# Kernel tuning notes

Hardware: AMD Instinct MI355X
Metric: run time of the kernel (lower is better)

Reference implementation:

```python
import jax, jax.numpy as jnp
import numpy as np

NODE_NUM = 256  # nodes per env block; N = NODE_NUM * n_thr
N, MAX_DEG, N_FEAT, N_HID, N_CLASS = 8192, 16, 128, 256, 64


def _xavier_uniform(key, fan_in, fan_out, gain=1.414):
    limit = gain * np.sqrt(6.0 / (fan_in + fan_out))
    return jax.random.uniform(key, (fan_in, fan_out), jnp.float32, -limit, limit)


def setup_inputs() -> dict:
    key = jax.random.key(0)
    k1, k2, k3, k4 = jax.random.split(key, 4)
    x = jax.random.normal(k1, (N, N_FEAT), jnp.float32)
    edge_index = jax.random.randint(k2, (N, MAX_DEG), 0, NODE_NUM)  # local neighbor ids, -1 = pad
    W1 = _xavier_uniform(k3, N_FEAT, N_HID)
    W2 = _xavier_uniform(k4, N_HID, N_CLASS)
    return {"x": x, "edge_index": edge_index, "W1": W1, "W2": W2}


def build_adj(edge_index, node_num):
    # Vectorized version of the nested-Python-loop to_adj scatter.
    n, d = edge_index.shape
    rows = jnp.broadcast_to(jnp.arange(n)[:, None], (n, d))  # [N, D]
    cols = edge_index + node_num * (rows // node_num)        # global neighbor index
    valid = (edge_index != -1).astype(jnp.float32)
    # .max with 0 for invalid entries is a no-op regardless of the (wrapped) index,
    # exactly reproducing "set adj[i, j_ind] = 1 only when j != -1".
    adj = jnp.zeros((n, n), jnp.float32).at[rows.ravel(), cols.ravel()].max(valid.ravel())
    return adj


def reference(x, edge_index, W1, W2):
    adj = build_adj(edge_index, NODE_NUM)            # [N, N]
    h = jax.nn.relu(adj @ (x @ W1))                  # gc1 + relu (dropout is identity at eval)
    out = adj @ (h @ W2)                             # gc2
    return jax.nn.log_softmax(out, axis=1)
```

## Files before the change

### kernel.cpp

```cpp
#include <hip/hip_runtime.h>
#include <math.h>

#define NNODES   8192
#define NODE_NUM 256
#define MAX_DEG  16
#define N_FEAT   128
#define N_HID    256
#define N_CLASS  64

#define AG_STRIDE 136
#define HB_STRIDE 264

typedef __attribute__((ext_vector_type(8))) short bf16x8;
typedef __attribute__((ext_vector_type(4))) float f32x4;

static __device__ __forceinline__ short f2b(float f) {
    unsigned u = __float_as_uint(f);
    unsigned r = (u + 0x7fffu + ((u >> 16) & 1u)) >> 16;
    return (short)r;
}

__global__ __launch_bounds__(512) void k_main(const float* __restrict__ x,
                                              const int* __restrict__ edge,
                                              const float* __restrict__ W1,
                                              const float* __restrict__ W2,
                                              unsigned int* __restrict__ maskw,
                                              float* __restrict__ t2) {
    __shared__ short agg[32 * AG_STRIDE];
    __shared__ short hb[32 * HB_STRIDE];

    const int bid  = blockIdx.x;
    const int work = (bid & 7) * 32 + (bid >> 3);
    const int row0 = work * 32;
    const int t    = threadIdx.x;
    const int w    = t >> 6, l = t & 63;
    const int l16  = l & 15, l4 = l >> 4;

    bf16x8 w1f[4][4];
    {
        const int ntb = (w & 3) * 4;
#pragma unroll
        for (int n = 0; n < 4; ++n)
#pragma unroll
            for (int k4 = 0; k4 < 4; ++k4) {
                const int col = (ntb + n) * 16 + l16;
                const int kb  = k4 * 32 + l4 * 8;
                bf16x8 v;
#pragma unroll
                for (int j = 0; j < 8; ++j) v[j] = f2b(W1[(kb + j) * N_HID + col]);
                w1f[n][k4] = v;
            }
    }
    bf16x8 w2f[8];
    {
        const int col = (w & 3) * 16 + l16;
#pragma unroll
        for (int k8 = 0; k8 < 8; ++k8) {
            const int kb = k8 * 32 + l4 * 8;
            bf16x8 v;
#pragma unroll
            for (int j = 0; j < 8; ++j) v[j] = f2b(W2[(kb + j) * N_CLASS + col]);
            w2f[k8] = v;
        }
    }

    {
        const int r = t >> 4, c = t & 15;
        const int node = row0 + r;
        const int base = node & ~(NODE_NUM - 1);
        const int* e = edge + (size_t)node * MAX_DEG;
        int ids[MAX_DEG];
#pragma unroll
        for (int k = 0; k < MAX_DEG; ++k) ids[k] = e[k];
        unsigned m = 0;
#pragma unroll
        for (int k = 0; k < MAX_DEG; ++k) {
            bool skip = (ids[k] == -1);
#pragma unroll
            for (int q = 0; q < k; ++q) skip = skip || (ids[q] == ids[k]);
            if (!skip) m |= 1u << k;
        }
        if (c == 0) maskw[node] = m;
        float a[8] = {0, 0, 0, 0, 0, 0, 0, 0};
#pragma unroll
        for (int k = 0; k < MAX_DEG; ++k) {
            if (m & (1u << k)) {
                const float* rowp = x + (size_t)(base + ids[k]) * N_FEAT + c * 8;
                float4 v0 = *(const float4*)(rowp);
                float4 v1 = *(const float4*)(rowp + 4);
                a[0] += v0.x; a[1] += v0.y; a[2] += v0.z; a[3] += v0.w;
                a[4] += v1.x; a[5] += v1.y; a[6] += v1.z; a[7] += v1.w;
            }
        }
        bf16x8 p;
#pragma unroll
        for (int j = 0; j < 8; ++j) p[j] = f2b(a[j]);
        *(bf16x8*)(&agg[r * AG_STRIDE + c * 8]) = p;
    }
    __syncthreads();

    const int mt = w >> 2, ntc = w & 3;
    {
        bf16x8 af[4];
#pragma unroll
        for (int k4 = 0; k4 < 4; ++k4)
            af[k4] = *(const bf16x8*)(&agg[(mt * 16 + l16) * AG_STRIDE + k4 * 32 + l4 * 8]);
#pragma unroll
        for (int n = 0; n < 4; ++n) {
            f32x4 acc = {0.f, 0.f, 0.f, 0.f};
#pragma unroll
            for (int k4 = 0; k4 < 4; ++k4)
                acc = __builtin_amdgcn_mfma_f32_16x16x32_bf16(af[k4], w1f[n][k4], acc, 0, 0, 0);
#pragma unroll
            for (int r = 0; r < 4; ++r)
                hb[(mt * 16 + l4 * 4 + r) * HB_STRIDE + (ntc * 4 + n) * 16 + l16] =
                    f2b(fmaxf(acc[r], 0.f));
        }
    }
    __syncthreads();

    {
        f32x4 acc = {0.f, 0.f, 0.f, 0.f};
#pragma unroll
        for (int k8 = 0; k8 < 8; ++k8) {
            bf16x8 a = *(const bf16x8*)(&hb[(mt * 16 + l16) * HB_STRIDE + k8 * 32 + l4 * 8]);
            acc = __builtin_amdgcn_mfma_f32_16x16x32_bf16(a, w2f[k8], acc, 0, 0, 0);
        }
#pragma unroll
        for (int r = 0; r < 4; ++r)
            t2[(size_t)(row0 + mt * 16 + l4 * 4 + r) * N_CLASS + ntc * 16 + l16] = acc[r];
    }
}

__global__ __launch_bounds__(512) void k_final(const float* __restrict__ t2,
                                               const int* __restrict__ edge,
                                               const unsigned int* __restrict__ maskw,
                                               float* __restrict__ out) {
    const int bid  = blockIdx.x;
    const int work = (bid & 7) * 32 + (bid >> 3);
    const int row0 = work * 32;
    const int t    = threadIdx.x;
    const int r = t >> 4, c = t & 15;
    const int node = row0 + r;
    const int base = node & ~(NODE_NUM - 1);
    const int* e = edge + (size_t)node * MAX_DEG;
    const unsigned m = maskw[node];

    float4 acc = {0.f, 0.f, 0.f, 0.f};
#pragma unroll
    for (int k = 0; k < MAX_DEG; ++k) {
        if (m & (1u << k)) {
            float4 v = *(const float4*)(t2 + (size_t)(base + e[k]) * N_CLASS + c * 4);
            acc.x += v.x; acc.y += v.y; acc.z += v.z; acc.w += v.w;
        }
    }
    float mx = fmaxf(fmaxf(acc.x, acc.y), fmaxf(acc.z, acc.w));
#pragma unroll
    for (int o = 1; o < 16; o <<= 1) mx = fmaxf(mx, __shfl_xor(mx, o, 64));
    float s = expf(acc.x - mx) + expf(acc.y - mx) + expf(acc.z - mx) + expf(acc.w - mx);
#pragma unroll
    for (int o = 1; o < 16; o <<= 1) s += __shfl_xor(s, o, 64);
    const float lse = mx + logf(s);

    float4 o4 = {acc.x - lse, acc.y - lse, acc.z - lse, acc.w - lse};
    *(float4*)(out + (size_t)node * N_CLASS + c * 4) = o4;
}

extern "C" void kernel_launch(void* const* d_in, const int* in_sizes, int n_in,
                              void* d_out, int out_size, void* d_ws, size_t ws_size,
                              hipStream_t stream) {
    const float* x    = (const float*)d_in[0];
    const int*   edge = (const int*)d_in[1];
    const float* W1   = (const float*)d_in[2];
    const float* W2   = (const float*)d_in[3];
    float* out = (float*)d_out;

    char* ws = (char*)d_ws;
    unsigned int* maskw = (unsigned int*)ws;
    float*        t2    = (float*)(ws + (64 << 10));

    k_main <<<NNODES / 32, 512, 0, stream>>>(x, edge, W1, W2, maskw, t2);
    k_final<<<NNODES / 32, 512, 0, stream>>>(t2, edge, maskw, out);
}
```

Baseline: 79.22 us.

## Pre-pack bf16 weight fragments and masks in a prep kernel, store t2 as bf16

Adds a prep kernel that computes the neighbor dedup masks and converts W1/W2 into bf16 MFMA fragment layout once. Each main-kernel block then loads its weight fragments with vector loads instead of strided scalar fp32 loads plus per-element conversion. The intermediate t2 is stored in bf16, halving its traffic, and the final kernel gathers 8 bf16 values per thread. The cost is an extra kernel launch and serialization between kernels, plus reduced precision in t2.

```diff
diff --git a/kernel.cpp b/kernel.cpp
--- a/kernel.cpp
+++ b/kernel.cpp
@@ -19,13 +19,48 @@
     unsigned r = (u + 0x7fffu + ((u >> 16) & 1u)) >> 16;
     return (short)r;
 }
-
-__global__ __launch_bounds__(512) void k_main(const float* __restrict__ x,
-                                              const int* __restrict__ edge,
+static __device__ __forceinline__ float b2f(short s) {
+    return __uint_as_float(((unsigned)(unsigned short)s) << 16);
+}
+
+__global__ __launch_bounds__(256) void k_prep(const int* __restrict__ edge,
                                               const float* __restrict__ W1,
                                               const float* __restrict__ W2,
                                               unsigned int* __restrict__ maskw,
-                                              float* __restrict__ t2) {
+                                              short* __restrict__ W1T,
+                                              short* __restrict__ W2T) {
+    const int g = blockIdx.x * 256 + threadIdx.x;
+    if (g < 8192) {
+        const int* e = edge + (size_t)g * MAX_DEG;
+        int ids[MAX_DEG];
+#pragma unroll
+        for (int k = 0; k < MAX_DEG; ++k) ids[k] = e[k];
+        unsigned m = 0;
+#pragma unroll
+        for (int k = 0; k < MAX_DEG; ++k) {
+            bool skip = (ids[k] == -1);
+#pragma unroll
+            for (int q = 0; q < k; ++q) skip = skip || (ids[q] == ids[k]);
+            if (!skip) m |= 1u << k;
+        }
+        maskw[g] = m;
+    } else if (g < 40960) {
+        const int o = g - 8192;
+        const int j = o & 7, l = (o >> 3) & 63, k4 = (o >> 9) & 3, nt = (o >> 11) & 15;
+        W1T[o] = f2b(W1[(k4 * 32 + (l >> 4) * 8 + j) * N_HID + nt * 16 + (l & 15)]);
+    } else if (g < 57344) {
+        const int o = g - 40960;
+        const int j = o & 7, l = (o >> 3) & 63, k8 = (o >> 9) & 7, nt = (o >> 12) & 3;
+        W2T[o] = f2b(W2[(k8 * 32 + (l >> 4) * 8 + j) * N_CLASS + nt * 16 + (l & 15)]);
+    }
+}
+
+__global__ __launch_bounds__(512) void k_main(const float* __restrict__ x,
+                                              const int* __restrict__ edge,
+                                              const unsigned int* __restrict__ maskw,
+                                              const short* __restrict__ W1T,
+                                              const short* __restrict__ W2T,
+                                              short* __restrict__ t2b) {
     __shared__ short agg[32 * AG_STRIDE];
     __shared__ short hb[32 * HB_STRIDE];
 
@@ -42,26 +77,15 @@
 #pragma unroll
         for (int n = 0; n < 4; ++n)
 #pragma unroll
-            for (int k4 = 0; k4 < 4; ++k4) {
-                const int col = (ntb + n) * 16 + l16;
-                const int kb  = k4 * 32 + l4 * 8;
-                bf16x8 v;
-#pragma unroll
-                for (int j = 0; j < 8; ++j) v[j] = f2b(W1[(kb + j) * N_HID + col]);
-                w1f[n][k4] = v;
-            }
+            for (int k4 = 0; k4 < 4; ++k4)
+                w1f[n][k4] = *(const bf16x8*)(W1T + ((size_t)((ntb + n) * 4 + k4) * 64 + l) * 8);
     }
     bf16x8 w2f[8];
     {
-        const int col = (w & 3) * 16 + l16;
-#pragma unroll
-        for (int k8 = 0; k8 < 8; ++k8) {
-            const int kb = k8 * 32 + l4 * 8;
-            bf16x8 v;
-#pragma unroll
-            for (int j = 0; j < 8; ++j) v[j] = f2b(W2[(kb + j) * N_CLASS + col]);
-            w2f[k8] = v;
-        }
+        const int nt = w & 3;
+#pragma unroll
+        for (int k8 = 0; k8 < 8; ++k8)
+            w2f[k8] = *(const bf16x8*)(W2T + ((size_t)(nt * 8 + k8) * 64 + l) * 8);
     }
 
     {
@@ -69,23 +93,12 @@
         const int node = row0 + r;
         const int base = node & ~(NODE_NUM - 1);
         const int* e = edge + (size_t)node * MAX_DEG;
-        int ids[MAX_DEG];
-#pragma unroll
-        for (int k = 0; k < MAX_DEG; ++k) ids[k] = e[k];
-        unsigned m = 0;
-#pragma unroll
-        for (int k = 0; k < MAX_DEG; ++k) {
-            bool skip = (ids[k] == -1);
-#pragma unroll
-            for (int q = 0; q < k; ++q) skip = skip || (ids[q] == ids[k]);
-            if (!skip) m |= 1u << k;
-        }
-        if (c == 0) maskw[node] = m;
+        const unsigned m = maskw[node];
         float a[8] = {0, 0, 0, 0, 0, 0, 0, 0};
 #pragma unroll
         for (int k = 0; k < MAX_DEG; ++k) {
             if (m & (1u << k)) {
-                const float* rowp = x + (size_t)(base + ids[k]) * N_FEAT + c * 8;
+                const float* rowp = x + (size_t)(base + e[k]) * N_FEAT + c * 8;
                 float4 v0 = *(const float4*)(rowp);
                 float4 v1 = *(const float4*)(rowp + 4);
                 a[0] += v0.x; a[1] += v0.y; a[2] += v0.z; a[3] += v0.w;
@@ -128,11 +141,11 @@
         }
 #pragma unroll
         for (int r = 0; r < 4; ++r)
-            t2[(size_t)(row0 + mt * 16 + l4 * 4 + r) * N_CLASS + ntc * 16 + l16] = acc[r];
-    }
-}
-
-__global__ __launch_bounds__(512) void k_final(const float* __restrict__ t2,
+            t2b[(size_t)(row0 + mt * 16 + l4 * 4 + r) * N_CLASS + ntc * 16 + l16] = f2b(acc[r]);
+    }
+}
+
+__global__ __launch_bounds__(256) void k_final(const short* __restrict__ t2b,
                                                const int* __restrict__ edge,
                                                const unsigned int* __restrict__ maskw,
                                                float* __restrict__ out) {
@@ -140,30 +153,38 @@
     const int work = (bid & 7) * 32 + (bid >> 3);
     const int row0 = work * 32;
     const int t    = threadIdx.x;
-    const int r = t >> 4, c = t & 15;
+    const int r = t >> 3, mm = t & 7;
     const int node = row0 + r;
     const int base = node & ~(NODE_NUM - 1);
     const int* e = edge + (size_t)node * MAX_DEG;
     const unsigned m = maskw[node];
 
-    float4 acc = {0.f, 0.f, 0.f, 0.f};
+    float acc[8] = {0, 0, 0, 0, 0, 0, 0, 0};
 #pragma unroll
     for (int k = 0; k < MAX_DEG; ++k) {
         if (m & (1u << k)) {
-            float4 v = *(const float4*)(t2 + (size_t)(base + e[k]) * N_CLASS + c * 4);
-            acc.x += v.x; acc.y += v.y; acc.z += v.z; acc.w += v.w;
-        }
-    }
-    float mx = fmaxf(fmaxf(acc.x, acc.y), fmaxf(acc.z, acc.w));
-#pragma unroll
-    for (int o = 1; o < 16; o <<= 1) mx = fmaxf(mx, __shfl_xor(mx, o, 64));
-    float s = expf(acc.x - mx) + expf(acc.y - mx) + expf(acc.z - mx) + expf(acc.w - mx);
-#pragma unroll
-    for (int o = 1; o < 16; o <<= 1) s += __shfl_xor(s, o, 64);
+            bf16x8 v = *(const bf16x8*)(t2b + (size_t)(base + e[k]) * N_CLASS + mm * 8);
+#pragma unroll
+            for (int j = 0; j < 8; ++j) acc[j] += b2f(v[j]);
+        }
+    }
+    float mx = acc[0];
+#pragma unroll
+    for (int j = 1; j < 8; ++j) mx = fmaxf(mx, acc[j]);
+#pragma unroll
+    for (int o = 1; o < 8; o <<= 1) mx = fmaxf(mx, __shfl_xor(mx, o, 64));
+    float s = 0.f;
+#pragma unroll
+    for (int j = 0; j < 8; ++j) s += expf(acc[j] - mx);
+#pragma unroll
+    for (int o = 1; o < 8; o <<= 1) s += __shfl_xor(s, o, 64);
     const float lse = mx + logf(s);
 
-    float4 o4 = {acc.x - lse, acc.y - lse, acc.z - lse, acc.w - lse};
-    *(float4*)(out + (size_t)node * N_CLASS + c * 4) = o4;
+    float* op = out + (size_t)node * N_CLASS + mm * 8;
+    float4 o0 = {acc[0] - lse, acc[1] - lse, acc[2] - lse, acc[3] - lse};
+    float4 o1 = {acc[4] - lse, acc[5] - lse, acc[6] - lse, acc[7] - lse};
+    *(float4*)(op)     = o0;
+    *(float4*)(op + 4) = o1;
 }
 
 extern "C" void kernel_launch(void* const* d_in, const int* in_sizes, int n_in,
@@ -177,8 +198,11 @@
 
     char* ws = (char*)d_ws;
     unsigned int* maskw = (unsigned int*)ws;
-    float*        t2    = (float*)(ws + (64 << 10));
-
-    k_main <<<NNODES / 32, 512, 0, stream>>>(x, edge, W1, W2, maskw, t2);
-    k_final<<<NNODES / 32, 512, 0, stream>>>(t2, edge, maskw, out);
-}
+    short*        W1T   = (short*)(ws + (32 << 10));
+    short*        W2T   = (short*)(ws + (96 << 10));
+    short*        t2b   = (short*)(ws + (128 << 10));
+
+    k_prep <<<256,         256, 0, stream>>>(edge, W1, W2, maskw, W1T, W2T);
+    k_main <<<NNODES / 32, 512, 0, stream>>>(x, edge, maskw, W1T, W2T, t2b);
+    k_final<<<NNODES / 32, 256, 0, stream>>>(t2b, edge, maskw, out);
+}
```

Result: faster. 77.26 us (-2.5%).

## Fuse both GCN kernels with per-env grid barrier and bf16 intermediate

Applied to the files above, without the earlier changes.

Merges the two kernels into one, where the eight blocks of each 256-node env synchronize through an atomic counter barrier before the second aggregation and log-softmax. W1 and W2 are staged through LDS with coalesced float4 loads instead of strided global gathers, and the intermediate t2 is stored as bf16 to halve gather traffic. This removes the second launch and the mask round-trip. In exchange it adds a memset, relies on all blocks of an env being co-resident to avoid deadlock, and loses some precision in t2.

```diff
diff --git a/kernel.cpp b/kernel.cpp
--- a/kernel.cpp
+++ b/kernel.cpp
@@ -12,6 +12,7 @@
 #define HB_STRIDE 264
 
 typedef __attribute__((ext_vector_type(8))) short bf16x8;
+typedef __attribute__((ext_vector_type(4))) short s16x4;
 typedef __attribute__((ext_vector_type(4))) float f32x4;
 
 static __device__ __forceinline__ short f2b(float f) {
@@ -19,60 +20,41 @@
     unsigned r = (u + 0x7fffu + ((u >> 16) & 1u)) >> 16;
     return (short)r;
 }
-
-__global__ __launch_bounds__(512) void k_main(const float* __restrict__ x,
-                                              const int* __restrict__ edge,
-                                              const float* __restrict__ W1,
-                                              const float* __restrict__ W2,
-                                              unsigned int* __restrict__ maskw,
-                                              float* __restrict__ t2) {
-    __shared__ short agg[32 * AG_STRIDE];
-    __shared__ short hb[32 * HB_STRIDE];
+static __device__ __forceinline__ float b2f(short s) {
+    return __uint_as_float(((unsigned)(unsigned short)s) << 16);
+}
+
+__global__ __launch_bounds__(512) void k_one(const float* __restrict__ x,
+                                             const int* __restrict__ edge,
+                                             const float* __restrict__ W1,
+                                             const float* __restrict__ W2,
+                                             short* __restrict__ t2b,
+                                             unsigned int* __restrict__ bar,
+                                             float* __restrict__ out) {
+    __shared__ __align__(16) char smem[131072];
+    float* w1s = (float*)smem;
+    float* w2s = (float*)smem;
+    short* agg = (short*)smem;
+    short* hb  = (short*)(smem + 32 * AG_STRIDE * 2);
 
     const int bid  = blockIdx.x;
     const int work = (bid & 7) * 32 + (bid >> 3);
     const int row0 = work * 32;
+    const int env  = work >> 3;
     const int t    = threadIdx.x;
     const int w    = t >> 6, l = t & 63;
     const int l16  = l & 15, l4 = l >> 4;
 
-    bf16x8 w1f[4][4];
+    const int r = t >> 4, c = t & 15;
+    const int node = row0 + r;
+    const int base = node & ~(NODE_NUM - 1);
+    const int* e = edge + (size_t)node * MAX_DEG;
+
+    unsigned m = 0;
     {
-        const int ntb = (w & 3) * 4;
-#pragma unroll
-        for (int n = 0; n < 4; ++n)
-#pragma unroll
-            for (int k4 = 0; k4 < 4; ++k4) {
-                const int col = (ntb + n) * 16 + l16;
-                const int kb  = k4 * 32 + l4 * 8;
-                bf16x8 v;
-#pragma unroll
-                for (int j = 0; j < 8; ++j) v[j] = f2b(W1[(kb + j) * N_HID + col]);
-                w1f[n][k4] = v;
-            }
-    }
-    bf16x8 w2f[8];
-    {
-        const int col = (w & 3) * 16 + l16;
-#pragma unroll
-        for (int k8 = 0; k8 < 8; ++k8) {
-            const int kb = k8 * 32 + l4 * 8;
-            bf16x8 v;
-#pragma unroll
-            for (int j = 0; j < 8; ++j) v[j] = f2b(W2[(kb + j) * N_CLASS + col]);
-            w2f[k8] = v;
-        }
-    }
-
-    {
-        const int r = t >> 4, c = t & 15;
-        const int node = row0 + r;
-        const int base = node & ~(NODE_NUM - 1);
-        const int* e = edge + (size_t)node * MAX_DEG;
         int ids[MAX_DEG];
 #pragma unroll
         for (int k = 0; k < MAX_DEG; ++k) ids[k] = e[k];
-        unsigned m = 0;
 #pragma unroll
         for (int k = 0; k < MAX_DEG; ++k) {
             bool skip = (ids[k] == -1);
@@ -80,7 +62,6 @@
             for (int q = 0; q < k; ++q) skip = skip || (ids[q] == ids[k]);
             if (!skip) m |= 1u << k;
         }
-        if (c == 0) maskw[node] = m;
         float a[8] = {0, 0, 0, 0, 0, 0, 0, 0};
 #pragma unroll
         for (int k = 0; k < MAX_DEG; ++k) {
@@ -92,78 +73,121 @@
                 a[4] += v1.x; a[5] += v1.y; a[6] += v1.z; a[7] += v1.w;
             }
         }
-        bf16x8 p;
-#pragma unroll
-        for (int j = 0; j < 8; ++j) p[j] = f2b(a[j]);
-        *(bf16x8*)(&agg[r * AG_STRIDE + c * 8]) = p;
+
+        {
+            const float4* s4 = (const float4*)W1;
+            float4* d4 = (float4*)w1s;
+#pragma unroll
+            for (int i = 0; i < 16; ++i) d4[i * 512 + t] = s4[i * 512 + t];
+        }
+        __syncthreads();
+        bf16x8 w1f[4][4];
+        {
+            const int ntb = (w & 3) * 4;
+#pragma unroll
+            for (int n = 0; n < 4; ++n)
+#pragma unroll
+                for (int k4 = 0; k4 < 4; ++k4) {
+                    bf16x8 v;
+#pragma unroll
+                    for (int j = 0; j < 8; ++j)
+                        v[j] = f2b(w1s[(k4 * 32 + l4 * 8 + j) * N_HID + (ntb + n) * 16 + l16]);
+                    w1f[n][k4] = v;
+                }
+        }
+        __syncthreads();
+        {
+            const float4* s4 = (const float4*)W2;
+            float4* d4 = (float4*)w2s;
+#pragma unroll
+            for (int i = 0; i < 8; ++i) d4[i * 512 + t] = s4[i * 512 + t];
+        }
+        __syncthreads();
+        bf16x8 w2f[8];
+        {
+            const int nt = w & 3;
+#pragma unroll
+            for (int k8 = 0; k8 < 8; ++k8) {
+                bf16x8 v;
+#pragma unroll
+                for (int j = 0; j < 8; ++j)
+                    v[j] = f2b(w2s[(k8 * 32 + l4 * 8 + j) * N_CLASS + nt * 16 + l16]);
+                w2f[k8] = v;
+            }
+        }
+        __syncthreads();
+
+        {
+            bf16x8 p;
+#pragma unroll
+            for (int j = 0; j < 8; ++j) p[j] = f2b(a[j]);
+            *(bf16x8*)(agg + r * AG_STRIDE + c * 8) = p;
+        }
+        __syncthreads();
+
+        const int mt = w >> 2, ntc = w & 3;
+        {
+            bf16x8 af[4];
+#pragma unroll
+            for (int k4 = 0; k4 < 4; ++k4)
+                af[k4] = *(const bf16x8*)(agg + (mt * 16 + l16) * AG_STRIDE + k4 * 32 + l4 * 8);
+#pragma unroll
+            for (int n = 0; n < 4; ++n) {
+                f32x4 acc = {0.f, 0.f, 0.f, 0.f};
+#pragma unroll
+                for (int k4 = 0; k4 < 4; ++k4)
+                    acc = __builtin_amdgcn_mfma_f32_16x16x32_bf16(af[k4], w1f[n][k4], acc, 0, 0, 0);
+#pragma unroll
+                for (int rr = 0; rr < 4; ++rr)
+                    hb[(mt * 16 + l4 * 4 + rr) * HB_STRIDE + (ntc * 4 + n) * 16 + l16] =
+                        f2b(fmaxf(acc[rr], 0.f));
+            }
+        }
+        __syncthreads();
+
+        {
+            f32x4 acc = {0.f, 0.f, 0.f, 0.f};
+#pragma unroll
+            for (int k8 = 0; k8 < 8; ++k8) {
+                bf16x8 av = *(const bf16x8*)(hb + (mt * 16 + l16) * HB_STRIDE + k8 * 32 + l4 * 8);
+                acc = __builtin_amdgcn_mfma_f32_16x16x32_bf16(av, w2f[k8], acc, 0, 0, 0);
+            }
+#pragma unroll
+            for (int rr = 0; rr < 4; ++rr)
+                t2b[(size_t)(row0 + mt * 16 + l4 * 4 + rr) * N_CLASS + ntc * 16 + l16] =
+                    f2b(acc[rr]);
+        }
+    }
+
+    __threadfence();
+    __syncthreads();
+    if (t == 0) {
+        __hip_atomic_fetch_add(&bar[env], 1u, __ATOMIC_ACQ_REL, __HIP_MEMORY_SCOPE_AGENT);
+        while (__hip_atomic_load(&bar[env], __ATOMIC_ACQUIRE, __HIP_MEMORY_SCOPE_AGENT) < 8u)
+            __builtin_amdgcn_s_sleep(2);
     }
     __syncthreads();
-
-    const int mt = w >> 2, ntc = w & 3;
+    __threadfence();
+
     {
-        bf16x8 af[4];
-#pragma unroll
-        for (int k4 = 0; k4 < 4; ++k4)
-            af[k4] = *(const bf16x8*)(&agg[(mt * 16 + l16) * AG_STRIDE + k4 * 32 + l4 * 8]);
-#pragma unroll
-        for (int n = 0; n < 4; ++n) {
-            f32x4 acc = {0.f, 0.f, 0.f, 0.f};
-#pragma unroll
-            for (int k4 = 0; k4 < 4; ++k4)
-                acc = __builtin_amdgcn_mfma_f32_16x16x32_bf16(af[k4], w1f[n][k4], acc, 0, 0, 0);
-#pragma unroll
-            for (int r = 0; r < 4; ++r)
-                hb[(mt * 16 + l4 * 4 + r) * HB_STRIDE + (ntc * 4 + n) * 16 + l16] =
-                    f2b(fmaxf(acc[r], 0.f));
-        }
+        float a0 = 0.f, a1 = 0.f, a2 = 0.f, a3 = 0.f;
+#pragma unroll
+        for (int k = 0; k < MAX_DEG; ++k) {
+            if (m & (1u << k)) {
+                s16x4 v = *(const s16x4*)(t2b + (size_t)(base + e[k]) * N_CLASS + c * 4);
+                a0 += b2f(v[0]); a1 += b2f(v[1]); a2 += b2f(v[2]); a3 += b2f(v[3]);
+            }
+        }
+        float mx = fmaxf(fmaxf(a0, a1), fmaxf(a2, a3));
+#pragma unroll
+        for (int o = 1; o < 16; o <<= 1) mx = fmaxf(mx, __shfl_xor(mx, o, 64));
+        float s = expf(a0 - mx) + expf(a1 - mx) + expf(a2 - mx) + expf(a3 - mx);
+#pragma unroll
+        for (int o = 1; o < 16; o <<= 1) s += __shfl_xor(s, o, 64);
+        const float lse = mx + logf(s);
+        float4 o4 = {a0 - lse, a1 - lse, a2 - lse, a3 - lse};
+        *(float4*)(out + (size_t)node * N_CLASS + c * 4) = o4;
     }
-    __syncthreads();
-
-    {
-        f32x4 acc = {0.f, 0.f, 0.f, 0.f};
-#pragma unroll
-        for (int k8 = 0; k8 < 8; ++k8) {
-            bf16x8 a = *(const bf16x8*)(&hb[(mt * 16 + l16) * HB_STRIDE + k8 * 32 + l4 * 8]);
-            acc = __builtin_amdgcn_mfma_f32_16x16x32_bf16(a, w2f[k8], acc, 0, 0, 0);
-        }
-#pragma unroll
-        for (int r = 0; r < 4; ++r)
-            t2[(size_t)(row0 + mt * 16 + l4 * 4 + r) * N_CLASS + ntc * 16 + l16] = acc[r];
-    }
-}
-
-__global__ __launch_bounds__(512) void k_final(const float* __restrict__ t2,
-                                               const int* __restrict__ edge,
-                                               const unsigned int* __restrict__ maskw,
-                                               float* __restrict__ out) {
-    const int bid  = blockIdx.x;
-    const int work = (bid & 7) * 32 + (bid >> 3);
-    const int row0 = work * 32;
-    const int t    = threadIdx.x;
-    const int r = t >> 4, c = t & 15;
-    const int node = row0 + r;
-    const int base = node & ~(NODE_NUM - 1);
-    const int* e = edge + (size_t)node * MAX_DEG;
-    const unsigned m = maskw[node];
-
-    float4 acc = {0.f, 0.f, 0.f, 0.f};
-#pragma unroll
-    for (int k = 0; k < MAX_DEG; ++k) {
-        if (m & (1u << k)) {
-            float4 v = *(const float4*)(t2 + (size_t)(base + e[k]) * N_CLASS + c * 4);
-            acc.x += v.x; acc.y += v.y; acc.z += v.z; acc.w += v.w;
-        }
-    }
-    float mx = fmaxf(fmaxf(acc.x, acc.y), fmaxf(acc.z, acc.w));
-#pragma unroll
-    for (int o = 1; o < 16; o <<= 1) mx = fmaxf(mx, __shfl_xor(mx, o, 64));
-    float s = expf(acc.x - mx) + expf(acc.y - mx) + expf(acc.z - mx) + expf(acc.w - mx);
-#pragma unroll
-    for (int o = 1; o < 16; o <<= 1) s += __shfl_xor(s, o, 64);
-    const float lse = mx + logf(s);
-
-    float4 o4 = {acc.x - lse, acc.y - lse, acc.z - lse, acc.w - lse};
-    *(float4*)(out + (size_t)node * N_CLASS + c * 4) = o4;
 }
 
 extern "C" void kernel_launch(void* const* d_in, const int* in_sizes, int n_in,
@@ -176,9 +200,9 @@
     float* out = (float*)d_out;
 
     char* ws = (char*)d_ws;
-    unsigned int* maskw = (unsigned int*)ws;
-    float*        t2    = (float*)(ws + (64 << 10));
-
-    k_main <<<NNODES / 32, 512, 0, stream>>>(x, edge, W1, W2, maskw, t2);
-    k_final<<<NNODES / 32, 512, 0, stream>>>(t2, edge, maskw, out);
-}
+    short*        t2b = (short*)ws;
+    unsigned int* bar = (unsigned int*)(ws + (1 << 20));
+
+    (void)hipMemsetAsync(bar, 0, 32 * sizeof(unsigned int), stream);
+    k_one<<<NNODES / 32, 512, 0, stream>>>(x, edge, W1, W2, t2b, bar, out);
+}
```

Result: slower. 169.3 us (+113.7%).
